# Kernel optimization log

Measured on AMD Instinct MI355X. Metric: run time of the kernel, lower is better.

The kernel has to match this reference:

```python
import jax, jax.numpy as jnp
import numpy as np

K = 32  # sae_k

def setup_inputs() -> dict:
    key = jax.random.key(0)
    k1, k2, k3 = jax.random.split(key, 3)
    B, D, H = 8192, 256, 8192  # batch, d_in, hidden_dim = d_in * scale_size
    x = jax.random.normal(k1, (B, D), dtype=jnp.float32)
    W_enc = jax.random.normal(k2, (H, D), dtype=jnp.float32) * (1.0 / np.sqrt(D))
    b_enc = jnp.zeros((H,), dtype=jnp.float32)
    # W_dec initialized as clone of encoder weight then row-normalized to unit norm
    W_dec = jax.random.normal(k3, (H, D), dtype=jnp.float32)
    W_dec = W_dec / (jnp.linalg.norm(W_dec, axis=1, keepdims=True) + jnp.finfo(jnp.float32).eps)
    b_dec = jnp.zeros((D,), dtype=jnp.float32)
    return {"x": x, "W_enc": W_enc, "b_enc": b_enc, "W_dec": W_dec, "b_dec": b_dec}

def reference(x, W_enc, b_enc, W_dec, b_dec):
    # sae_in = x - b_dec; pre_acts = relu(encoder(sae_in))
    sae_in = x - b_dec
    pre_acts = jax.nn.relu(jnp.einsum('bd,hd->bh', sae_in, W_enc) + b_enc)  # [B, H]
    # top-k activation: keep k largest latents per row, zero the rest
    topk_vals, topk_idx = jax.lax.top_k(pre_acts, K)  # [B, K]
    B = pre_acts.shape[0]
    rows = jnp.arange(B)[:, None]
    z = jnp.zeros_like(pre_acts).at[rows, topk_idx].set(topk_vals)  # sparse activation [B, H]
    # decode
    x_reconstructed = jnp.einsum('bh,hd->bd', z, W_dec) + b_dec
    return x_reconstructed
```

## Files before the change

### kernel.cpp

```cpp
#include <hip/hip_runtime.h>

#define DIN   256
#define HID   8192
#define BATCH 8192
#define TOPK  32
#define BM    32
#define HHALF 4096
#define NCH   16
#define NS1   48
#define MRG   96
#define NS2   40
#define AS_LD 264
#define XF_LD 260
#define CAP   112
#define K2_LD 113
#define WCAP  352
#define THRM  0.1375f
#define DBM   4
#define DT    256
#define GK_OFF ((size_t)4 << 20)

typedef __bf16 bf16x8 __attribute__((ext_vector_type(8)));
typedef unsigned short u16x8 __attribute__((ext_vector_type(8)));
typedef float f32x4v __attribute__((ext_vector_type(4)));

__device__ __forceinline__ unsigned short f2bf(float f) {
  unsigned x = __builtin_bit_cast(unsigned, f);
  x = x + 0x7fffu + ((x >> 16) & 1u);
  return (unsigned short)(x >> 16);
}

__global__ __launch_bounds__(512) void wenc_cast(
    const float* __restrict__ Wenc, unsigned short* __restrict__ wsb)
{
  const int g = (int)blockIdx.x * 512 + (int)threadIdx.x;
  const int h = g >> 5, u = g & 31, kg = u >> 2, quad = u & 3;
  const float* src = Wenc + (size_t)h * DIN + kg * 32 + quad * 8;
  float4 a = *(const float4*)src;
  float4 b = *(const float4*)(src + 4);
  u16x8 o;
  o[0] = f2bf(a.x); o[1] = f2bf(a.y); o[2] = f2bf(a.z); o[3] = f2bf(a.w);
  o[4] = f2bf(b.x); o[5] = f2bf(b.y); o[6] = f2bf(b.z); o[7] = f2bf(b.w);
  *(u16x8*)(wsb + ((size_t)(((h >> 4) * 8 + kg) * 64 + quad * 16 + (h & 15))) * 8) = o;
}

__global__ __launch_bounds__(512) __attribute__((amdgpu_waves_per_eu(4)))
void sae_enc(
    const float* __restrict__ x,    const float* __restrict__ benc,
    const float* __restrict__ bdec, const unsigned short* __restrict__ wsb,
    unsigned* __restrict__ gkeys)
{
  __shared__ __align__(16) union UA {
    unsigned short As[BM][AS_LD];
    struct { unsigned wkey[8][WCAP]; unsigned char wrow[8][WCAP]; } w;
  } ua;
  __shared__ unsigned keys2[BM][K2_LD];
  __shared__ __align__(16) float benc_l[HHALF];
  __shared__ int   cnt[BM];
  __shared__ float rthr[BM];
  __shared__ int   wn[8];

  const int tid  = (int)threadIdx.x;
  const int wave = tid >> 6;
  const int lane = tid & 63;
  const int quad = lane >> 4;
  const int ln15 = lane & 15;
  const int rt   = (int)blockIdx.x >> 1;
  const int hs   = (int)blockIdx.x & 1;
  const int mb   = rt * BM;

  {
    const int r = tid >> 4, seg = tid & 15;
    const float* xs = x + (size_t)(mb + r) * DIN + seg * 16;
    const float* bs = bdec + seg * 16;
    float ss = 0.0f;
    #pragma unroll
    for (int j = 0; j < 4; ++j) {
      float4 xv = *(const float4*)(xs + 4 * j);
      float4 bv = *(const float4*)(bs + 4 * j);
      float dx = xv.x - bv.x, dy = xv.y - bv.y;
      float dz = xv.z - bv.z, dw = xv.w - bv.w;
      ss += dx * dx + dy * dy + dz * dz + dw * dw;
      unsigned short* dst = &ua.As[r][seg * 16 + 4 * j];
      dst[0] = f2bf(dx); dst[1] = f2bf(dy);
      dst[2] = f2bf(dz); dst[3] = f2bf(dw);
    }
    #pragma unroll
    for (int d = 1; d < 16; d <<= 1) ss += __shfl_xor(ss, d, 16);
    if (seg == 0) { rthr[r] = THRM * sqrtf(ss); cnt[r] = 0; }
  }
  {
    const float* bsrc = benc + hs * HHALF + tid * 8;
    float4 b0 = *(const float4*)bsrc;
    float4 b1 = *(const float4*)(bsrc + 4);
    *(float4*)&benc_l[tid * 8]     = b0;
    *(float4*)&benc_l[tid * 8 + 4] = b1;
  }
  __syncthreads();

  bf16x8 afrag[2][8];
  #pragma unroll
  for (int mt = 0; mt < 2; ++mt)
    #pragma unroll
    for (int gk = 0; gk < 8; ++gk)
      afrag[mt][gk] = *(const bf16x8*)&ua.As[mt * 16 + ln15][gk * 32 + quad * 8];

  float thr[8];
  #pragma unroll
  for (int s = 0; s < 8; ++s) thr[s] = rthr[(s >> 2) * 16 + quad * 4 + (s & 3)];
  __syncthreads();

  unsigned wbase = 0;

  for (int c = 0; c < NCH; ++c) {
    const unsigned short* bp =
        wsb + (((size_t)(hs * 256 + c * 16 + wave * 2) * 512) + lane) * 8;
    #pragma unroll
    for (int nt = 0; nt < 2; ++nt) {
      bf16x8 bfrag[8];
      #pragma unroll
      for (int kg = 0; kg < 8; ++kg)
        bfrag[kg] = *(const bf16x8*)(bp + (size_t)nt * 4096 + (size_t)kg * 512);

      const int hwl = c * 256 + (wave * 2 + nt) * 16 + ln15;
      const float be = benc_l[hwl];
      f32x4v acc[2];
      #pragma unroll
      for (int mt = 0; mt < 2; ++mt)
        #pragma unroll
        for (int i = 0; i < 4; ++i) acc[mt][i] = be;

      #pragma unroll
      for (int kg = 0; kg < 8; ++kg) {
        acc[0] = __builtin_amdgcn_mfma_f32_16x16x32_bf16(afrag[0][kg], bfrag[kg], acc[0], 0, 0, 0);
        acc[1] = __builtin_amdgcn_mfma_f32_16x16x32_bf16(afrag[1][kg], bfrag[kg], acc[1], 0, 0, 0);
      }

      const unsigned idxpart = (unsigned)(8191 - (hs * HHALF + hwl));
      #pragma unroll
      for (int s = 0; s < 8; ++s) {
        const int mt = s >> 2, i = s & 3;
        const bool take = acc[mt][i] > thr[s];
        const unsigned long long bm = __ballot(take);
        if (take) {
          const int pos = (int)wbase + __popcll(bm & ((1ull << lane) - 1ull));
          if (pos < WCAP) {
            ua.w.wkey[wave][pos] = ((unsigned)f2bf(acc[mt][i]) << 16) | idxpart;
            ua.w.wrow[wave][pos] = (unsigned char)(mt * 16 + quad * 4 + i);
          }
        }
        wbase += (unsigned)__popcll(bm);
      }
    }
  }
  if (lane == 0) wn[wave] = (int)(wbase < WCAP ? wbase : WCAP);
  __syncthreads();

  for (int w = 0; w < 8; ++w) {
    const int n = wn[w];
    for (int e = tid; e < n; e += 512) {
      const unsigned k = ua.w.wkey[w][e];
      const int row = (int)ua.w.wrow[w][e];
      const int sl = atomicAdd(&cnt[row], 1);
      if (sl < CAP) keys2[row][sl] = k;
    }
  }
  __syncthreads();

  {
    const int row = tid >> 4, l16 = tid & 15;
    const int n = min(cnt[row], CAP);
    unsigned myk[CAP / 16];
    int rk[CAP / 16];
    #pragma unroll
    for (int j = 0; j < CAP / 16; ++j) {
      const int idx = l16 + 16 * j;
      myk[j] = (idx < n) ? keys2[row][idx] : 0u;
      rk[j] = 0;
    }
    for (int e = 0; e < n; ++e) {
      const unsigned k2 = keys2[row][e];
      #pragma unroll
      for (int j = 0; j < CAP / 16; ++j) rk[j] += (k2 > myk[j]) ? 1 : 0;
    }
    unsigned* gout = gkeys + (size_t)(mb + row) * MRG + hs * NS1;
    #pragma unroll
    for (int j = 0; j < CAP / 16; ++j) {
      const int idx = l16 + 16 * j;
      if (idx < n && rk[j] < NS1) gout[rk[j]] = myk[j];
    }
    if (l16 == 0)
      for (int p = n; p < NS1; ++p) gout[p] = (unsigned)(0x4000 + hs * 64 + p);
  }
}

__global__ __launch_bounds__(DT) void sae_dec(
    const float* __restrict__ x,    const float* __restrict__ Wenc,
    const float* __restrict__ benc, const float* __restrict__ Wdec,
    const float* __restrict__ bdec, const unsigned* __restrict__ gkeys,
    float* __restrict__ out)
{
  __shared__ unsigned mk[DBM][MRG];
  __shared__ __align__(16) float xf[DBM][XF_LD];
  __shared__ float tv[DBM][NS2];
  __shared__ int   ti[DBM][NS2];
  __shared__ float sv[DBM][TOPK];
  __shared__ int   si[DBM][TOPK];

  const int tid = (int)threadIdx.x;
  const int mb  = (int)blockIdx.x * DBM;

  #pragma unroll
  for (int i = tid; i < DBM * MRG; i += DT)
    mk[i / MRG][i % MRG] = gkeys[(size_t)mb * MRG + i];

  {
    const int r = tid >> 6, seg = tid & 63;
    float4 xv = *(const float4*)(x + (size_t)(mb + r) * DIN + seg * 4);
    float4 bv = *(const float4*)(bdec + seg * 4);
    float4 d;
    d.x = xv.x - bv.x; d.y = xv.y - bv.y; d.z = xv.z - bv.z; d.w = xv.w - bv.w;
    *(float4*)&xf[r][seg * 4] = d;
  }
  __syncthreads();

  if (tid < DBM * 32) {
    const int row = tid >> 5, l32 = tid & 31;
    unsigned myk[3];
    int rk[3];
    #pragma unroll
    for (int j = 0; j < 3; ++j) { myk[j] = mk[row][l32 + 32 * j]; rk[j] = 0; }
    for (int e = 0; e < MRG; ++e) {
      const unsigned k2 = mk[row][e];
      #pragma unroll
      for (int j = 0; j < 3; ++j) rk[j] += (k2 > myk[j]) ? 1 : 0;
    }
    #pragma unroll
    for (int j = 0; j < 3; ++j)
      if (rk[j] < NS2) ti[row][rk[j]] = 8191 - (int)(myk[j] & 0xFFFFu);
  }
  __syncthreads();

  {
    const int sub = tid & 15, task = tid >> 4;
    for (int p = 0; p < (DBM * NS2) / 16; ++p) {
      const int pp = p * 16 + task;
      const int row = pp / NS2, cand = pp - row * NS2;
      const int h = ti[row][cand];
      double a0 = 0.0, a1 = 0.0;
      if (h >= 0) {
        const float* wp = Wenc + (size_t)h * DIN + sub * 16;
        const float* xp = &xf[row][sub * 16];
        float4 w0 = *(const float4*)(wp);
        float4 w1 = *(const float4*)(wp + 4);
        float4 w2 = *(const float4*)(wp + 8);
        float4 w3 = *(const float4*)(wp + 12);
        float4 x0 = *(const float4*)(xp);
        float4 x1 = *(const float4*)(xp + 4);
        float4 x2 = *(const float4*)(xp + 8);
        float4 x3 = *(const float4*)(xp + 12);
        a0 += (double)x0.x * (double)w0.x + (double)x0.y * (double)w0.y;
        a1 += (double)x0.z * (double)w0.z + (double)x0.w * (double)w0.w;
        a0 += (double)x1.x * (double)w1.x + (double)x1.y * (double)w1.y;
        a1 += (double)x1.z * (double)w1.z + (double)x1.w * (double)w1.w;
        a0 += (double)x2.x * (double)w2.x + (double)x2.y * (double)w2.y;
        a1 += (double)x2.z * (double)w2.z + (double)x2.w * (double)w2.w;
        a0 += (double)x3.x * (double)w3.x + (double)x3.y * (double)w3.y;
        a1 += (double)x3.z * (double)w3.z + (double)x3.w * (double)w3.w;
      }
      double accd = a0 + a1;
      accd += __shfl_xor(accd, 8, 16);
      accd += __shfl_xor(accd, 4, 16);
      accd += __shfl_xor(accd, 2, 16);
      accd += __shfl_xor(accd, 1, 16);
      if (sub == 0) {
        float ev = (h >= 0) ? ((float)accd + benc[h]) : 0.0f;
        ev = ev > 0.0f ? ev : 0.0f;
        tv[row][cand] = ev;
      }
    }
  }
  __syncthreads();

  if (tid < DBM * NS2) {
    const int row = tid / NS2, cand = tid - row * NS2;
    const float v = tv[row][cand];
    const int   h = ti[row][cand];
    int rk = 0;
    for (int e = 0; e < NS2; ++e) {
      const float v2 = tv[row][e];
      const int   h2 = ti[row][e];
      rk += (v2 > v || (v2 == v && (unsigned)h2 < (unsigned)h)) ? 1 : 0;
    }
    if (rk < TOPK) { sv[row][rk] = v; si[row][rk] = h; }
  }
  __syncthreads();

  {
    const int r = tid >> 6, d0 = (tid & 63) * 4;
    float4 bb = *(const float4*)(bdec + d0);
    float o0 = bb.x, o1 = bb.y, o2 = bb.z, o3 = bb.w;
    #pragma unroll
    for (int s = 0; s < TOPK; ++s) {
      const float v = sv[r][s];
      const int   h = si[r][s];
      const float* wp = Wdec + (size_t)((v > 0.0f) ? h : 0) * DIN + d0;
      float4 w = *(const float4*)wp;
      o0 += v * w.x; o1 += v * w.y; o2 += v * w.z; o3 += v * w.w;
    }
    float4 o;
    o.x = o0; o.y = o1; o.z = o2; o.w = o3;
    *(float4*)(out + (size_t)(mb + r) * DIN + d0) = o;
  }
}

extern "C" void kernel_launch(void* const* d_in, const int* in_sizes, int n_in,
                              void* d_out, int out_size, void* d_ws, size_t ws_size,
                              hipStream_t stream) {
  const float* x    = (const float*)d_in[0];
  const float* Wenc = (const float*)d_in[1];
  const float* benc = (const float*)d_in[2];
  const float* Wdec = (const float*)d_in[3];
  const float* bdec = (const float*)d_in[4];
  float* out = (float*)d_out;
  unsigned short* wsb = (unsigned short*)d_ws;
  unsigned* gkeys = (unsigned*)((char*)d_ws + GK_OFF);

  wenc_cast<<<dim3((HID * DIN / 8) / 512), dim3(512), 0, stream>>>(Wenc, wsb);
  sae_enc<<<dim3(2 * BATCH / BM), dim3(512), 0, stream>>>(x, benc, bdec, wsb, gkeys);
  sae_dec<<<dim3(BATCH / DBM), dim3(DT), 0, stream>>>(x, Wenc, benc, Wdec, bdec, gkeys, out);
}
```

Baseline: 197.2 us.

## Double-buffer encoder weight fragments and raise MFMA priority in the encode loop

```diff
diff --git a/kernel.cpp b/kernel.cpp
--- a/kernel.cpp
+++ b/kernel.cpp
@@ -44,7 +44,9 @@
   *(u16x8*)(wsb + ((size_t)(((h >> 4) * 8 + kg) * 64 + quad * 16 + (h & 15))) * 8) = o;
 }
 
-__global__ __launch_bounds__(512) __attribute__((amdgpu_waves_per_eu(4)))
+#define TOFF(t) ((size_t)((((t) >> 1) * 16) + ((t) & 1)) * 4096)
+
+__global__ __launch_bounds__(512) __attribute__((amdgpu_waves_per_eu(3)))
 void sae_enc(
     const float* __restrict__ x,    const float* __restrict__ benc,
     const float* __restrict__ bdec, const unsigned short* __restrict__ wsb,
@@ -111,48 +113,62 @@
   __syncthreads();
 
   unsigned wbase = 0;
-
-  for (int c = 0; c < NCH; ++c) {
-    const unsigned short* bp =
-        wsb + (((size_t)(hs * 256 + c * 16 + wave * 2) * 512) + lane) * 8;
-    #pragma unroll
-    for (int nt = 0; nt < 2; ++nt) {
-      bf16x8 bfrag[8];
-      #pragma unroll
-      for (int kg = 0; kg < 8; ++kg)
-        bfrag[kg] = *(const bf16x8*)(bp + (size_t)nt * 4096 + (size_t)kg * 512);
-
-      const int hwl = c * 256 + (wave * 2 + nt) * 16 + ln15;
-      const float be = benc_l[hwl];
-      f32x4v acc[2];
-      #pragma unroll
-      for (int mt = 0; mt < 2; ++mt)
-        #pragma unroll
-        for (int i = 0; i < 4; ++i) acc[mt][i] = be;
-
-      #pragma unroll
-      for (int kg = 0; kg < 8; ++kg) {
-        acc[0] = __builtin_amdgcn_mfma_f32_16x16x32_bf16(afrag[0][kg], bfrag[kg], acc[0], 0, 0, 0);
-        acc[1] = __builtin_amdgcn_mfma_f32_16x16x32_bf16(afrag[1][kg], bfrag[kg], acc[1], 0, 0, 0);
-      }
-
-      const unsigned idxpart = (unsigned)(8191 - (hs * HHALF + hwl));
-      #pragma unroll
-      for (int s = 0; s < 8; ++s) {
-        const int mt = s >> 2, i = s & 3;
-        const bool take = acc[mt][i] > thr[s];
-        const unsigned long long bm = __ballot(take);
-        if (take) {
-          const int pos = (int)wbase + __popcll(bm & ((1ull << lane) - 1ull));
-          if (pos < WCAP) {
-            ua.w.wkey[wave][pos] = ((unsigned)f2bf(acc[mt][i]) << 16) | idxpart;
-            ua.w.wrow[wave][pos] = (unsigned char)(mt * 16 + quad * 4 + i);
-          }
-        }
-        wbase += (unsigned)__popcll(bm);
-      }
-    }
-  }
+  const unsigned short* wbp =
+      wsb + (((size_t)(hs * 256 + wave * 2) * 512) + lane) * 8;
+
+#define ENC_TILE(tt, B)                                                      \
+  {                                                                          \
+    const int hwl = ((tt) >> 1) * 256 + (wave * 2 + ((tt) & 1)) * 16 + ln15; \
+    const float be = benc_l[hwl];                                            \
+    f32x4v acc[2];                                                           \
+    _Pragma("unroll")                                                        \
+    for (int mt = 0; mt < 2; ++mt)                                           \
+      _Pragma("unroll")                                                      \
+      for (int i = 0; i < 4; ++i) acc[mt][i] = 0.0f;                         \
+    __builtin_amdgcn_s_setprio(1);                                           \
+    _Pragma("unroll")                                                        \
+    for (int kg = 0; kg < 8; ++kg) {                                         \
+      acc[0] = __builtin_amdgcn_mfma_f32_16x16x32_bf16(afrag[0][kg], B[kg], acc[0], 0, 0, 0); \
+      acc[1] = __builtin_amdgcn_mfma_f32_16x16x32_bf16(afrag[1][kg], B[kg], acc[1], 0, 0, 0); \
+    }                                                                        \
+    __builtin_amdgcn_s_setprio(0);                                           \
+    const unsigned idxpart = (unsigned)(8191 - (hs * HHALF + hwl));          \
+    _Pragma("unroll")                                                        \
+    for (int s = 0; s < 8; ++s) {                                            \
+      const int mt = s >> 2, i = s & 3;                                      \
+      const float v = acc[mt][i] + be;                                       \
+      const bool take = v > thr[s];                                          \
+      const unsigned long long bmk = __ballot(take);                         \
+      if (take) {                                                            \
+        const int pos = (int)wbase + __popcll(bmk & ((1ull << lane) - 1ull));\
+        if (pos < WCAP) {                                                    \
+          ua.w.wkey[wave][pos] = ((unsigned)f2bf(v) << 16) | idxpart;        \
+          ua.w.wrow[wave][pos] = (unsigned char)(mt * 16 + quad * 4 + i);    \
+        }                                                                    \
+      }                                                                      \
+      wbase += (unsigned)__popcll(bmk);                                      \
+    }                                                                        \
+  }
+
+#define ENC_LOAD(tt, B)                                                      \
+  _Pragma("unroll")                                                          \
+  for (int kg = 0; kg < 8; ++kg)                                             \
+    B[kg] = *(const bf16x8*)(wbp + TOFF(tt) + (size_t)kg * 512);
+
+  {
+    bf16x8 bA[8], bB[8];
+    ENC_LOAD(0, bA);
+    for (int t = 0; t < 32; t += 2) {
+      ENC_LOAD(t + 1, bB);
+      ENC_TILE(t, bA);
+      const int tn = (t + 2 < 32) ? t + 2 : 30;
+      ENC_LOAD(tn, bA);
+      ENC_TILE(t + 1, bB);
+    }
+  }
+#undef ENC_TILE
+#undef ENC_LOAD
+
   if (lane == 0) wn[wave] = (int)(wbase < WCAP ? wbase : WCAP);
   __syncthreads();
 
```

Result: slower. 201.7 us (+2.3%).
